# Performance work log

Hardware: AMD Instinct MI355X
Metric: run time of the kernel (lower is better)

The kernel has to match this reference:

```python
import jax, jax.numpy as jnp
import numpy as np

D_MODEL = 1024
H = 16
D_K = D_MODEL // H  # 64


def setup_inputs() -> dict:
    key = jax.random.key(0)
    ks = jax.random.split(key, 10)
    B, S = 4, 4096
    q = jax.random.normal(ks[0], (B, S, D_MODEL), dtype=jnp.float32)
    k = jax.random.normal(ks[1], (B, S, D_MODEL), dtype=jnp.float32)
    v = jax.random.normal(ks[2], (B, S, D_MODEL), dtype=jnp.float32)
    m = jax.random.uniform(ks[3], (B, S), dtype=jnp.float32)
    sc = 1.0 / np.sqrt(D_MODEL)
    Wq = jax.random.uniform(ks[4], (D_MODEL, D_K), jnp.float32, -sc, sc)
    bq = jax.random.uniform(ks[5], (D_K,), jnp.float32, -sc, sc)
    Wk = jax.random.uniform(ks[6], (D_MODEL, D_K), jnp.float32, -sc, sc)
    bk = jax.random.uniform(ks[7], (D_K,), jnp.float32, -sc, sc)
    Wv = jax.random.uniform(ks[8], (D_MODEL, D_K), jnp.float32, -sc, sc)
    bv = jax.random.uniform(ks[9], (D_K,), jnp.float32, -sc, sc)
    return {"q": q, "k": k, "v": v, "m": m,
            "Wq": Wq, "bq": bq, "Wk": Wk, "bk": bk, "Wv": Wv, "bv": bv}


def reference(q, k, v, m, Wq, bq, Wk, bk, Wv, bv):
    # single-head projections: [B,S,d_model] -> [B,S,d_k]
    qh = q @ Wq + bq
    kh = k @ Wk + bk
    vh = v @ Wv + bv
    # scaled dot-product scores [B,S,S]
    a = jnp.einsum("bqd,bkd->bqk", qh, kh) / jnp.sqrt(jnp.float32(D_K))
    # multiplicative per-query-row mask BEFORE softmax (non-standard variant)
    a = a * m[:, :, None]
    a = jax.nn.softmax(a, axis=-1)
    # AV: [B,S,S] x [B,S,d_k] -> [B,S,d_k]
    y = jnp.einsum("bqk,bkd->bqd", a, vh)
    return y
```

## Files before the change

kernel.cpp:

```cpp
#include <hip/hip_runtime.h>


typedef __attribute__((ext_vector_type(8))) short short8;
typedef __attribute__((ext_vector_type(4))) float float4v;
typedef __attribute__((ext_vector_type(4))) unsigned int uint4v;

#define DEV static __device__ __forceinline__

DEV unsigned short f2bf(float f) {
  unsigned int x; __builtin_memcpy(&x, &f, 4);
  x += 0x7fff + ((x >> 16) & 1);
  return (unsigned short)(x >> 16);
}

__global__ __launch_bounds__(256) void transpose_w(
    const float* __restrict__ Wq, const float* __restrict__ Wk,
    const float* __restrict__ Wv, unsigned short* __restrict__ WT) {
  int idx = blockIdx.x * 256 + threadIdx.x;
  int p = idx >> 16;
  int r = idx & 65535;
  int kk = r >> 6, d = r & 63;
  const float* W = (p == 0) ? Wq : (p == 1) ? Wk : Wv;
  WT[p * 65536 + d * 1024 + kk] = f2bf(W[r]);
}

__global__ __launch_bounds__(256) void proj_kernel(
    const float* __restrict__ xq, const float* __restrict__ xk,
    const float* __restrict__ xv, const float* __restrict__ mmask,
    const float* __restrict__ bq, const float* __restrict__ bk,
    const float* __restrict__ bv, const unsigned short* __restrict__ WT,
    unsigned short* __restrict__ qs, unsigned short* __restrict__ khh,
    unsigned short* __restrict__ vhT) {
  constexpr int LDSTR = 136;
  __shared__ __align__(16) unsigned short Xs[64 * LDSTR];
  __shared__ __align__(16) unsigned short Ws[64 * LDSTR];

  const int p = blockIdx.x >> 8;
  const int rt = blockIdx.x & 255;
  const int row0 = rt * 64;
  const int t = threadIdx.x;
  const int w = t >> 6, ln = t & 63;
  const int lr = ln & 15, quad = ln >> 4;

  const float* X = (p == 0) ? xq : (p == 1) ? xk : xv;
  const unsigned short* WTp = WT + p * 65536;
  const float* Xbase = X + (size_t)row0 * 1024;

  float4v acc[4];
#pragma unroll
  for (int i = 0; i < 4; ++i) acc[i] = (float4v){0.f, 0.f, 0.f, 0.f};

  const int srow = t >> 4;
  const int scol = (t & 15) * 8;

  float4v xr[4][2];
  uint4v wr[4];

#define ISSUE(kc_)                                                         \
  {                                                                        \
    const int k0_ = (kc_) * 128;                                           \
    _Pragma("unroll") for (int ps = 0; ps < 4; ++ps) {                     \
      const int rr = srow + ps * 16;                                       \
      const float* s_ = Xbase + (size_t)rr * 1024 + k0_ + scol;            \
      xr[ps][0] = *(const float4v*)s_;                                     \
      xr[ps][1] = *(const float4v*)(s_ + 4);                               \
      wr[ps] = *(const uint4v*)&WTp[(size_t)rr * 1024 + k0_ + scol];       \
    }                                                                      \
  }

  ISSUE(0);
  for (int kc = 0; kc < 8; ++kc) {
#pragma unroll
    for (int ps = 0; ps < 4; ++ps) {
      const int rr = srow + ps * 16;
      unsigned short tmp[8];
#pragma unroll
      for (int i = 0; i < 4; ++i) {
        tmp[i] = f2bf(xr[ps][0][i]);
        tmp[4 + i] = f2bf(xr[ps][1][i]);
      }
      __builtin_memcpy(&Xs[rr * LDSTR + scol], tmp, 16);
      *(uint4v*)&Ws[rr * LDSTR + scol] = wr[ps];
    }
    __syncthreads();
    if (kc < 7) ISSUE(kc + 1);

    if (p < 2) {
#pragma unroll
      for (int ks = 0; ks < 4; ++ks) {
        short8 af = *(const short8*)&Xs[(w * 16 + lr) * LDSTR + ks * 32 + quad * 8];
#pragma unroll
        for (int ct = 0; ct < 4; ++ct) {
          short8 bf = *(const short8*)&Ws[(ct * 16 + lr) * LDSTR + ks * 32 + quad * 8];
          acc[ct] = __builtin_amdgcn_mfma_f32_16x16x32_bf16(af, bf, acc[ct], 0, 0, 0);
        }
      }
    } else {
#pragma unroll
      for (int ks = 0; ks < 4; ++ks) {
        short8 af = *(const short8*)&Ws[(w * 16 + lr) * LDSTR + ks * 32 + quad * 8];
#pragma unroll
        for (int ct = 0; ct < 4; ++ct) {
          short8 bf = *(const short8*)&Xs[(ct * 16 + lr) * LDSTR + ks * 32 + quad * 8];
          acc[ct] = __builtin_amdgcn_mfma_f32_16x16x32_bf16(af, bf, acc[ct], 0, 0, 0);
        }
      }
    }
    __syncthreads();
  }
#undef ISSUE

  if (p == 0) {
    const float L2E8 = 1.4426950408889634f * 0.125f;
#pragma unroll
    for (int r = 0; r < 4; ++r) {
      int sg = row0 + w * 16 + quad * 4 + r;
      float mv = mmask[sg] * L2E8;
#pragma unroll
      for (int ct = 0; ct < 4; ++ct) {
        int d = ct * 16 + lr;
        qs[(size_t)sg * 64 + d] = f2bf((acc[ct][r] + bq[d]) * mv);
      }
    }
  } else if (p == 1) {
#pragma unroll
    for (int r = 0; r < 4; ++r) {
      int sg = row0 + w * 16 + quad * 4 + r;
#pragma unroll
      for (int ct = 0; ct < 4; ++ct) {
        int d = ct * 16 + lr;
        khh[(size_t)sg * 64 + d] = f2bf(acc[ct][r] + bk[d]);
      }
    }
  } else {
    int b = row0 >> 12, sloc = row0 & 4095;
#pragma unroll
    for (int r = 0; r < 4; ++r) {
      int d = w * 16 + quad * 4 + r;
      float bias = bv[d];
#pragma unroll
      for (int ct = 0; ct < 4; ++ct) {
        int sg = sloc + ct * 16 + lr;
        vhT[(size_t)b * 64 * 4096 + (size_t)d * 4096 + sg] = f2bf(acc[ct][r] + bias);
      }
    }
  }
}

#define SPLITS 4
__global__ __launch_bounds__(256) void attn_split(
    const unsigned short* __restrict__ qs, const unsigned short* __restrict__ khh,
    const unsigned short* __restrict__ vhT, float* __restrict__ O_part,
    float* __restrict__ L_part) {
  constexpr int LDSTR = 88;
  __shared__ __align__(16) unsigned short Ks[64 * LDSTR];
  __shared__ __align__(16) unsigned short Vs[64 * LDSTR];
  __shared__ __align__(16) unsigned short Ps[4 * 16 * LDSTR];

  const int split = blockIdx.x >> 8;
  const int rest  = blockIdx.x & 255;
  const int b = rest >> 6;
  const int s0 = (rest & 63) * 64;
  const int t = threadIdx.x, w = t >> 6, ln = t & 63;
  const int lr = ln & 15, quad = ln >> 4;

  const size_t qrow = (size_t)(b * 4096 + s0 + w * 16 + lr) * 64;
  short8 qf0 = *(const short8*)&qs[qrow + quad * 8];
  short8 qf1 = *(const short8*)&qs[qrow + 32 + quad * 8];

  float Lacc[4] = {0.f, 0.f, 0.f, 0.f};
  float4v O[4];
#pragma unroll
  for (int i = 0; i < 4; ++i) O[i] = (float4v){0.f, 0.f, 0.f, 0.f};

  const int srow = t >> 3, scol = (t & 7) * 8;
  const unsigned short* Kg = khh + (size_t)b * 4096 * 64;
  const unsigned short* Vg = vhT + (size_t)b * 64 * 4096;
  unsigned short* Pw = Ps + w * 16 * LDSTR;

  uint4v kr[2], vr[2];

#define ISSUE_KV(kt_)                                                       \
  {                                                                         \
    const int k0_ = split * 1024 + (kt_) * 64;                              \
    _Pragma("unroll") for (int ps = 0; ps < 2; ++ps) {                      \
      const int rr = srow + ps * 32;                                        \
      kr[ps] = *(const uint4v*)&Kg[(size_t)(k0_ + rr) * 64 + scol];         \
      vr[ps] = *(const uint4v*)&Vg[(size_t)rr * 4096 + k0_ + scol];         \
    }                                                                       \
  }

  ISSUE_KV(0);
  for (int kt = 0; kt < 16; ++kt) {
#pragma unroll
    for (int ps = 0; ps < 2; ++ps) {
      const int rr = srow + ps * 32;
      *(uint4v*)&Ks[rr * LDSTR + scol] = kr[ps];
      *(uint4v*)&Vs[rr * LDSTR + scol] = vr[ps];
    }
    __syncthreads();
    if (kt < 15) ISSUE_KV(kt + 1);

    float4v sc[4];
#pragma unroll
    for (int ct = 0; ct < 4; ++ct) {
      sc[ct] = (float4v){0.f, 0.f, 0.f, 0.f};
      short8 kf0 = *(const short8*)&Ks[(ct * 16 + lr) * LDSTR + quad * 8];
      short8 kf1 = *(const short8*)&Ks[(ct * 16 + lr) * LDSTR + 32 + quad * 8];
      sc[ct] = __builtin_amdgcn_mfma_f32_16x16x32_bf16(qf0, kf0, sc[ct], 0, 0, 0);
      sc[ct] = __builtin_amdgcn_mfma_f32_16x16x32_bf16(qf1, kf1, sc[ct], 0, 0, 0);
    }

#pragma unroll
    for (int ct = 0; ct < 4; ++ct)
#pragma unroll
      for (int r = 0; r < 4; ++r) {
        float pv = exp2f(sc[ct][r]);
        Lacc[r] += pv;
        Pw[(quad * 4 + r) * LDSTR + ct * 16 + lr] = f2bf(pv);
      }

    __asm__ volatile("s_waitcnt lgkmcnt(0)" ::: "memory");

    short8 pf0 = *(const short8*)&Pw[lr * LDSTR + quad * 8];
    short8 pf1 = *(const short8*)&Pw[lr * LDSTR + 32 + quad * 8];
#pragma unroll
    for (int dt = 0; dt < 4; ++dt) {
      short8 vf0 = *(const short8*)&Vs[(dt * 16 + lr) * LDSTR + quad * 8];
      short8 vf1 = *(const short8*)&Vs[(dt * 16 + lr) * LDSTR + 32 + quad * 8];
      O[dt] = __builtin_amdgcn_mfma_f32_16x16x32_bf16(pf0, vf0, O[dt], 0, 0, 0);
      O[dt] = __builtin_amdgcn_mfma_f32_16x16x32_bf16(pf1, vf1, O[dt], 0, 0, 0);
    }
    __syncthreads();
  }
#undef ISSUE_KV

#pragma unroll
  for (int r = 0; r < 4; ++r) {
    float s = Lacc[r];
    s += __shfl_xor(s, 1);
    s += __shfl_xor(s, 2);
    s += __shfl_xor(s, 4);
    s += __shfl_xor(s, 8);
    Lacc[r] = s;
  }

#pragma unroll
  for (int r = 0; r < 4; ++r) {
    int prow = b * 4096 + s0 + w * 16 + quad * 4 + r;
    size_t obase = ((size_t)split * 16384 + prow) * 64;
#pragma unroll
    for (int dt = 0; dt < 4; ++dt)
      O_part[obase + dt * 16 + lr] = O[dt][r];
    if (lr == 0) L_part[(size_t)split * 16384 + prow] = Lacc[r];
  }
}

__global__ __launch_bounds__(256) void attn_reduce(
    const float* __restrict__ O_part, const float* __restrict__ L_part,
    float* __restrict__ out) {
  size_t idx = (size_t)blockIdx.x * 256 + threadIdx.x;
  size_t row = idx >> 6;
  float l = L_part[row] + L_part[16384 + row] + L_part[2 * 16384 + row] +
            L_part[3 * 16384 + row];
  float o = O_part[idx] + O_part[idx + (size_t)16384 * 64] +
            O_part[idx + (size_t)2 * 16384 * 64] +
            O_part[idx + (size_t)3 * 16384 * 64];
  out[idx] = o / l;
}

extern "C" void kernel_launch(void* const* d_in, const int* in_sizes, int n_in,
                              void* d_out, int out_size, void* d_ws, size_t ws_size,
                              hipStream_t stream) {
  const float* q  = (const float*)d_in[0];
  const float* k  = (const float*)d_in[1];
  const float* v  = (const float*)d_in[2];
  const float* m  = (const float*)d_in[3];
  const float* Wq = (const float*)d_in[4];
  const float* bq = (const float*)d_in[5];
  const float* Wk = (const float*)d_in[6];
  const float* bk = (const float*)d_in[7];
  const float* Wv = (const float*)d_in[8];
  const float* bv = (const float*)d_in[9];
  float* out = (float*)d_out;

  unsigned short* ws16 = (unsigned short*)d_ws;
  unsigned short* WT  = ws16;
  unsigned short* qs  = WT + 3 * 65536;
  unsigned short* kh  = qs + 16384 * 64;
  unsigned short* vhT = kh + 16384 * 64;
  float* O_part = (float*)(vhT + 16384 * 64);
  float* L_part = O_part + (size_t)SPLITS * 16384 * 64;

  transpose_w<<<dim3(768), dim3(256), 0, stream>>>(Wq, Wk, Wv, WT);
  proj_kernel<<<dim3(768), dim3(256), 0, stream>>>(q, k, v, m, bq, bk, bv, WT,
                                                   qs, kh, vhT);
  attn_split<<<dim3(SPLITS * 256), dim3(256), 0, stream>>>(qs, kh, vhT,
                                                           O_part, L_part);
  attn_reduce<<<dim3(4096), dim3(256), 0, stream>>>(O_part, L_part, out);
}
```

Baseline: 261.6 us.

## Drop LDS staging in projection; each wave loads MFMA fragments from global

The projection kernel now gives each wave its own 16-row tile and loads X and bf16 W fragments straight from global memory into MFMA operands. This removes the shared-memory staging, both block barriers and the register double-buffering. Because W is now fetched by every wave instead of shared across a 64-row block, W traffic grows, and the loads no longer overlap compute through explicit prefetch. The V-transposed output layout is adjusted to match the new per-wave tile mapping.

Measured after the change: 289.7 us. +10.7%, slower.

```diff
diff --git a/kernel.cpp b/kernel.cpp
--- a/kernel.cpp
+++ b/kernel.cpp
@@ -31,90 +31,57 @@
     const float* __restrict__ bv, const unsigned short* __restrict__ WT,
     unsigned short* __restrict__ qs, unsigned short* __restrict__ khh,
     unsigned short* __restrict__ vhT) {
-  constexpr int LDSTR = 136;
-  __shared__ __align__(16) unsigned short Xs[64 * LDSTR];
-  __shared__ __align__(16) unsigned short Ws[64 * LDSTR];
-
-  const int p = blockIdx.x >> 8;
-  const int rt = blockIdx.x & 255;
-  const int row0 = rt * 64;
   const int t = threadIdx.x;
   const int w = t >> 6, ln = t & 63;
   const int lr = ln & 15, quad = ln >> 4;
 
+  const int gw = blockIdx.x * 4 + w;
+  const int p = gw >> 10;
+  const int row0 = (gw & 1023) * 16;
+
   const float* X = (p == 0) ? xq : (p == 1) ? xk : xv;
-  const unsigned short* WTp = WT + p * 65536;
-  const float* Xbase = X + (size_t)row0 * 1024;
+  const float* Xl = X + (size_t)(row0 + lr) * 1024 + quad * 8;
+  const unsigned short* Wl = WT + p * 65536 + (size_t)lr * 1024 + quad * 8;
 
   float4v acc[4];
 #pragma unroll
   for (int i = 0; i < 4; ++i) acc[i] = (float4v){0.f, 0.f, 0.f, 0.f};
 
-  const int srow = t >> 4;
-  const int scol = (t & 15) * 8;
-
-  float4v xr[4][2];
-  uint4v wr[4];
-
-#define ISSUE(kc_)                                                         \
-  {                                                                        \
-    const int k0_ = (kc_) * 128;                                           \
-    _Pragma("unroll") for (int ps = 0; ps < 4; ++ps) {                     \
-      const int rr = srow + ps * 16;                                       \
-      const float* s_ = Xbase + (size_t)rr * 1024 + k0_ + scol;            \
-      xr[ps][0] = *(const float4v*)s_;                                     \
-      xr[ps][1] = *(const float4v*)(s_ + 4);                               \
-      wr[ps] = *(const uint4v*)&WTp[(size_t)rr * 1024 + k0_ + scol];       \
-    }                                                                      \
-  }
-
-  ISSUE(0);
   for (int kc = 0; kc < 8; ++kc) {
 #pragma unroll
-    for (int ps = 0; ps < 4; ++ps) {
-      const int rr = srow + ps * 16;
-      unsigned short tmp[8];
-#pragma unroll
-      for (int i = 0; i < 4; ++i) {
-        tmp[i] = f2bf(xr[ps][0][i]);
-        tmp[4 + i] = f2bf(xr[ps][1][i]);
-      }
-      __builtin_memcpy(&Xs[rr * LDSTR + scol], tmp, 16);
-      *(uint4v*)&Ws[rr * LDSTR + scol] = wr[ps];
-    }
-    __syncthreads();
-    if (kc < 7) ISSUE(kc + 1);
-
-    if (p < 2) {
-#pragma unroll
-      for (int ks = 0; ks < 4; ++ks) {
-        short8 af = *(const short8*)&Xs[(w * 16 + lr) * LDSTR + ks * 32 + quad * 8];
-#pragma unroll
-        for (int ct = 0; ct < 4; ++ct) {
-          short8 bf = *(const short8*)&Ws[(ct * 16 + lr) * LDSTR + ks * 32 + quad * 8];
-          acc[ct] = __builtin_amdgcn_mfma_f32_16x16x32_bf16(af, bf, acc[ct], 0, 0, 0);
-        }
-      }
-    } else {
-#pragma unroll
-      for (int ks = 0; ks < 4; ++ks) {
-        short8 af = *(const short8*)&Ws[(w * 16 + lr) * LDSTR + ks * 32 + quad * 8];
-#pragma unroll
-        for (int ct = 0; ct < 4; ++ct) {
-          short8 bf = *(const short8*)&Xs[(ct * 16 + lr) * LDSTR + ks * 32 + quad * 8];
-          acc[ct] = __builtin_amdgcn_mfma_f32_16x16x32_bf16(af, bf, acc[ct], 0, 0, 0);
-        }
-      }
-    }
-    __syncthreads();
-  }
-#undef ISSUE
+    for (int ks = 0; ks < 4; ++ks) {
+      const int ko = kc * 128 + ks * 32;
+      float4v x0 = *(const float4v*)(Xl + ko);
+      float4v x1 = *(const float4v*)(Xl + ko + 4);
+      short8 wf0 = *(const short8*)(Wl + ko);
+      short8 wf1 = *(const short8*)(Wl + 16384 + ko);
+      short8 wf2 = *(const short8*)(Wl + 32768 + ko);
+      short8 wf3 = *(const short8*)(Wl + 49152 + ko);
+      short8 xf;
+#pragma unroll
+      for (int j = 0; j < 4; ++j) {
+        xf[j] = (short)f2bf(x0[j]);
+        xf[4 + j] = (short)f2bf(x1[j]);
+      }
+      if (p < 2) {
+        acc[0] = __builtin_amdgcn_mfma_f32_16x16x32_bf16(xf, wf0, acc[0], 0, 0, 0);
+        acc[1] = __builtin_amdgcn_mfma_f32_16x16x32_bf16(xf, wf1, acc[1], 0, 0, 0);
+        acc[2] = __builtin_amdgcn_mfma_f32_16x16x32_bf16(xf, wf2, acc[2], 0, 0, 0);
+        acc[3] = __builtin_amdgcn_mfma_f32_16x16x32_bf16(xf, wf3, acc[3], 0, 0, 0);
+      } else {
+        acc[0] = __builtin_amdgcn_mfma_f32_16x16x32_bf16(wf0, xf, acc[0], 0, 0, 0);
+        acc[1] = __builtin_amdgcn_mfma_f32_16x16x32_bf16(wf1, xf, acc[1], 0, 0, 0);
+        acc[2] = __builtin_amdgcn_mfma_f32_16x16x32_bf16(wf2, xf, acc[2], 0, 0, 0);
+        acc[3] = __builtin_amdgcn_mfma_f32_16x16x32_bf16(wf3, xf, acc[3], 0, 0, 0);
+      }
+    }
+  }
 
   if (p == 0) {
     const float L2E8 = 1.4426950408889634f * 0.125f;
 #pragma unroll
     for (int r = 0; r < 4; ++r) {
-      int sg = row0 + w * 16 + quad * 4 + r;
+      int sg = row0 + quad * 4 + r;
       float mv = mmask[sg] * L2E8;
 #pragma unroll
       for (int ct = 0; ct < 4; ++ct) {
@@ -125,7 +92,7 @@
   } else if (p == 1) {
 #pragma unroll
     for (int r = 0; r < 4; ++r) {
-      int sg = row0 + w * 16 + quad * 4 + r;
+      int sg = row0 + quad * 4 + r;
 #pragma unroll
       for (int ct = 0; ct < 4; ++ct) {
         int d = ct * 16 + lr;
@@ -135,15 +102,13 @@
   } else {
     int b = row0 >> 12, sloc = row0 & 4095;
 #pragma unroll
-    for (int r = 0; r < 4; ++r) {
-      int d = w * 16 + quad * 4 + r;
-      float bias = bv[d];
-#pragma unroll
-      for (int ct = 0; ct < 4; ++ct) {
-        int sg = sloc + ct * 16 + lr;
-        vhT[(size_t)b * 64 * 4096 + (size_t)d * 4096 + sg] = f2bf(acc[ct][r] + bias);
-      }
-    }
+    for (int ct = 0; ct < 4; ++ct)
+#pragma unroll
+      for (int r = 0; r < 4; ++r) {
+        int d = ct * 16 + quad * 4 + r;
+        vhT[(size_t)b * 64 * 4096 + (size_t)d * 4096 + sloc + lr] =
+            f2bf(acc[ct][r] + bv[d]);
+      }
   }
 }
 
```
